# Kernel tuning notes

Measured on AMD Instinct MI355X. Metric: run time of the kernel, lower is better.

## Reference

```python
import jax, jax.numpy as jnp
import numpy as np


def fft_conv(u, k):
    # u: (b, d, l) signal, k: (d, l) per-channel filter
    # Causal (linear) convolution via zero-padded FFT of size 2*l.
    # Matches torch fft_conv: rfft(k)/n * rfft(u), irfft(norm='forward')
    # which nets out to the standard unnormalized-forward / 1/n-inverse pair.
    seqlen = u.shape[-1]
    fft_size = 2 * seqlen
    k_f = jnp.fft.rfft(k, n=fft_size)            # (d, fft_size//2+1) complex
    u_f = jnp.fft.rfft(u, n=fft_size)            # (b, d, fft_size//2+1)
    y = jnp.fft.irfft(u_f * k_f, n=fft_size)[..., :seqlen]
    return y


def setup_inputs() -> dict:
    key = jax.random.key(0)
    k1, k2 = jax.random.split(key)
    b, l, d = 4, 8192, 1024
    x = jax.random.normal(k1, (b, l, d), dtype=jnp.float32)
    filt = jax.random.normal(k2, (d, l), dtype=jnp.float32)  # nn.Parameter(d_model, l_max)
    return {"x": x, "filt": filt}


def reference(x, filt):
    # x: (b, l, d) -> transpose to (b, d, l), fft conv, transpose back
    u = jnp.swapaxes(x, 1, 2)
    y = fft_conv(u, filt)
    y = jnp.swapaxes(y, 1, 2)
    return y.astype(x.dtype)
```

## Files before the change

### kernel.cpp

```cpp
#include <hip/hip_runtime.h>


#define M 8192
#define NTH 256
#define MAXP 17

__device__ __forceinline__ float2 cadd(float2 a, float2 b){ return make_float2(a.x+b.x, a.y+b.y); }
__device__ __forceinline__ float2 csub(float2 a, float2 b){ return make_float2(a.x-b.x, a.y-b.y); }
__device__ __forceinline__ float2 cmul(float2 a, float2 b){ return make_float2(a.x*b.x - a.y*b.y, a.x*b.y + a.y*b.x); }
__device__ __forceinline__ float2 conjf2(float2 a){ return make_float2(a.x, -a.y); }
__device__ __forceinline__ int rev13(int k){ return (int)(__brev((unsigned)k) >> 19); }
__device__ __forceinline__ int swz(int e){ return e ^ ((e >> 4) & 15) ^ ((e >> 8) & 15); }

static __device__ const float PI_F = 3.14159265358979323846f;

constexpr float CR_C[17] = {
  1.f, 0.98078528f, 0.92387953f, 0.83146961f, 0.70710678f,
  0.55557023f, 0.38268343f, 0.19509032f, 0.f, -0.19509032f,
  -0.38268343f, -0.55557023f, -0.70710678f, -0.83146961f,
  -0.92387953f, -0.98078528f, -1.f };
constexpr float CR_S[17] = {
  0.f, 0.19509032f, 0.38268343f, 0.55557023f, 0.70710678f,
  0.83146961f, 0.92387953f, 0.98078528f, 1.f, 0.98078528f,
  0.92387953f, 0.83146961f, 0.70710678f, 0.55557023f,
  0.38268343f, 0.19509032f, 0.f };

__device__ __forceinline__ float2 cmul_cr(float2 a, int idx, bool inv) {
  if (idx == 0) return a;
  const float c = CR_C[idx], s = CR_S[idx];
  if (!inv) return make_float2(a.x*c + a.y*s, a.y*c - a.x*s);
  return make_float2(a.x*c - a.y*s, a.x*s + a.y*c);
}

template<int HS, bool INV, bool FIRST_PAD, bool LAST_HALF>
__device__ __forceinline__ void fft5_regs(float2 (&p)[32], int r) {
  float s, c;
  const float th = PI_F * (float)r * (1.0f / (16.0f * (float)HS));
  __sincosf(INV ? th : -th, &s, &c);
  float2 w[5];
  w[0] = make_float2(c, s);
  w[1] = cmul(w[0], w[0]);
  w[2] = cmul(w[1], w[1]);
  w[3] = cmul(w[2], w[2]);
  w[4] = cmul(w[3], w[3]);
  if (!INV) {
#pragma unroll
    for (int st = 0; st < 5; ++st) {
      const int D = 16 >> st;
#pragma unroll
      for (int t0 = 0; t0 < 32; ++t0) {
        if ((t0 & D) == 0) {
          const int u = t0 & (D - 1);
          float2 a = p[t0];
          if (FIRST_PAD && st == 0) {
            p[t0 + D] = cmul_cr(cmul(a, w[0]), u, false);
          } else {
            float2 b = p[t0 + D];
            p[t0] = cadd(a, b);
            p[t0 + D] = cmul_cr(cmul(csub(a, b), w[st]), u * (16 / D), false);
          }
        }
      }
    }
  } else {
#pragma unroll
    for (int st = 0; st < 5; ++st) {
      const int D = 1 << st;
#pragma unroll
      for (int t0 = 0; t0 < 32; ++t0) {
        if ((t0 & D) == 0) {
          const int u = t0 & (D - 1);
          float2 b = cmul_cr(cmul(p[t0 + D], w[4 - st]), u * (16 / D), true);
          float2 a = p[t0];
          p[t0] = cadd(a, b);
          if (!(LAST_HALF && st == 4)) p[t0 + D] = csub(a, b);
        }
      }
    }
  }
}

template<int HS, bool INV>
__device__ __forceinline__ void pass5_lds(float2* L, int tid) {
  const int r = tid & (HS - 1);
  const int base = ((tid - r) << 5) + r;
  float2 p[32];
#pragma unroll
  for (int t = 0; t < 32; ++t) p[t] = L[swz(base + t * HS)];
  fft5_regs<HS, INV, false, false>(p, r);
#pragma unroll
  for (int t = 0; t < 32; ++t) L[swz(base + t * HS)] = p[t];
}

template<bool INV>
__device__ __forceinline__ void pass3_lds(float2* L, int tid) {
#pragma unroll
  for (int g = 0; g < 4; ++g) {
    const int base = tid * 32 + g * 8;
    float2 p[8];
#pragma unroll
    for (int t = 0; t < 8; ++t) p[t] = L[swz(base + t)];
    if (!INV) {
#pragma unroll
      for (int st = 0; st < 3; ++st) {
        const int D = 4 >> st;
#pragma unroll
        for (int t0 = 0; t0 < 8; ++t0) {
          if ((t0 & D) == 0) {
            const int u = t0 & (D - 1);
            float2 a = p[t0], b = p[t0 + D];
            p[t0] = cadd(a, b);
            p[t0 + D] = cmul_cr(csub(a, b), u * (16 / D), false);
          }
        }
      }
    } else {
#pragma unroll
      for (int st = 0; st < 3; ++st) {
        const int D = 1 << st;
#pragma unroll
        for (int t0 = 0; t0 < 8; ++t0) {
          if ((t0 & D) == 0) {
            const int u = t0 & (D - 1);
            float2 b = cmul_cr(p[t0 + D], u * (16 / D), true);
            float2 a = p[t0];
            p[t0] = cadd(a, b);
            p[t0 + D] = csub(a, b);
          }
        }
      }
    }
#pragma unroll
    for (int t = 0; t < 8; ++t) L[swz(base + t)] = p[t];
  }
}

__global__ __launch_bounds__(NTH, 2)
void filt_fft_kernel(const float* __restrict__ filt, float4* __restrict__ kf) {
  __shared__ float2 L[M];
  const int tid = threadIdx.x;
  const int d = blockIdx.x;
  const float* fp = filt + (size_t)d * 8192;
  {
    float2 p[32];
#pragma unroll
    for (int t = 0; t < 16; ++t) {
      int m = tid + t * NTH;
      p[t] = make_float2(fp[2*m], fp[2*m + 1]);
    }
#pragma unroll
    for (int t = 16; t < 32; ++t) p[t] = make_float2(0.f, 0.f);
    fft5_regs<256, false, true, false>(p, tid);
#pragma unroll
    for (int t = 0; t < 32; ++t) L[swz(tid + t * 256)] = p[t];
  }
  __syncthreads();
  pass5_lds<8, false>(L, tid);
  __syncthreads();
  pass3_lds<false>(L, tid);
  __syncthreads();
  float4* out = kf + (size_t)d * (M/2 + 1);
  for (int k = tid; k <= M/2; k += NTH) {
    int rk  = rev13(k);
    int rmk = rev13((M - k) & (M - 1));
    float2 Zk = L[swz(rk)], Zmk = L[swz(rmk)];
    float2 Ze = make_float2(0.5f*(Zk.x + Zmk.x), 0.5f*(Zk.y - Zmk.y));
    float2 t  = make_float2(Zk.x - Zmk.x, Zk.y + Zmk.y);
    float2 Zo = make_float2(0.5f*t.y, -0.5f*t.x);
    float s, c; __sincosf(-PI_F * (float)k * (1.0f/(float)M), &s, &c);
    float2 W = make_float2(c, s);
    float2 WZo = cmul(W, Zo);
    float2 Kk = cadd(Ze, WZo);
    float2 Km = conjf2(csub(Ze, WZo));
    out[k] = make_float4(Kk.x, Kk.y, Km.x, Km.y);
  }
}

__global__ __launch_bounds__(NTH, 2)
void longconv_kf_kernel(const float* __restrict__ x,
                        const float4* __restrict__ kf,
                        float* __restrict__ y) {
  __shared__ float2 L[M];
  const int tid = threadIdx.x;

  const int nwg = gridDim.x;
  const int cpx = nwg >> 3;
  const int bid = blockIdx.x;
  const int blk = (bid & 7) * cpx + (bid >> 3);
  const int d = blk & 1023;
  const int b = blk >> 10;

  {
    const float* xp = x + (size_t)b * (8192 * 1024) + d;
    float2 p[32];
#pragma unroll
    for (int t = 0; t < 16; ++t) {
      int m = tid + t * NTH;
      p[t] = make_float2(xp[(size_t)(2*m)     * 1024],
                         xp[(size_t)(2*m + 1) * 1024]);
    }
#pragma unroll
    for (int t = 16; t < 32; ++t) p[t] = make_float2(0.f, 0.f);
    fft5_regs<256, false, true, false>(p, tid);
#pragma unroll
    for (int t = 0; t < 32; ++t) L[swz(tid + t * 256)] = p[t];
  }
  __syncthreads();
  pass5_lds<8, false>(L, tid);
  __syncthreads();
  pass3_lds<false>(L, tid);
  __syncthreads();

  {
    const float4* kfp = kf + (size_t)d * (M/2 + 1);
#pragma unroll
    for (int pq = 0; pq < MAXP; ++pq) {
      int k = tid + pq * NTH;
      if (k <= M/2) {
        float4 kv = kfp[k];
        int rk  = rev13(k);
        int rmk = rev13((M - k) & (M - 1));
        float2 Zk = L[swz(rk)], Zmk = L[swz(rmk)];
        float2 Ze = make_float2(0.5f*(Zk.x + Zmk.x), 0.5f*(Zk.y - Zmk.y));
        float2 t  = make_float2(Zk.x - Zmk.x, Zk.y + Zmk.y);
        float2 Zo = make_float2(0.5f*t.y, -0.5f*t.x);
        float s, c; __sincosf(-PI_F * (float)k * (1.0f/(float)M), &s, &c);
        float2 W = make_float2(c, s);
        float2 WZo = cmul(W, Zo);
        float2 Uk  = cadd(Ze, WZo);
        float2 Umk = conjf2(csub(Ze, WZo));
        float2 Yk  = cmul(Uk,  make_float2(kv.x, kv.y));
        float2 Ymk = cmul(Umk, make_float2(kv.z, kv.w));
        float2 Ye  = make_float2(0.5f*(Yk.x + Ymk.x), 0.5f*(Yk.y - Ymk.y));
        float2 t2  = make_float2(0.5f*(Yk.x - Ymk.x), 0.5f*(Yk.y + Ymk.y));
        float2 Zoy = cmul(conjf2(W), t2);
        float2 Zyk  = make_float2(Ye.x - Zoy.y, Ye.y + Zoy.x);
        float2 Zymk = make_float2(Ye.x + Zoy.y, Zoy.x - Ye.y);
        L[swz(rk)]  = Zyk;
        L[swz(rmk)] = Zymk;
      }
    }
  }
  __syncthreads();

  pass3_lds<true>(L, tid);
  __syncthreads();
  pass5_lds<8, true>(L, tid);
  __syncthreads();

  {
    float2 p[32];
#pragma unroll
    for (int t = 0; t < 32; ++t) p[t] = L[swz(tid + t * 256)];
    fft5_regs<256, true, false, true>(p, tid);
    float* yp = y + (size_t)b * (8192 * 1024) + d;
    const float inv = 1.0f / (float)M;
#pragma unroll
    for (int t = 0; t < 16; ++t) {
      int m = tid + t * NTH;
      yp[(size_t)(2*m)     * 1024] = p[t].x * inv;
      yp[(size_t)(2*m + 1) * 1024] = p[t].y * inv;
    }
  }
}

__global__ __launch_bounds__(NTH, 2)
void longconv_fallback_kernel(const float* __restrict__ x,
                              const float* __restrict__ filt,
                              float* __restrict__ y) {
  __shared__ float2 L[M];
  const int tid = threadIdx.x;
  const int nwg = gridDim.x;
  const int cpx = nwg >> 3;
  const int bid = blockIdx.x;
  const int blk = (bid & 7) * cpx + (bid >> 3);
  const int d = blk & 1023;
  const int b = blk >> 10;

  float2 Kk[MAXP], Kmk[MAXP];

  {
    const float* fp = filt + (size_t)d * 8192;
    float2 p[32];
#pragma unroll
    for (int t = 0; t < 16; ++t) {
      int m = tid + t * NTH;
      p[t] = make_float2(fp[2*m], fp[2*m + 1]);
    }
#pragma unroll
    for (int t = 16; t < 32; ++t) p[t] = make_float2(0.f, 0.f);
    fft5_regs<256, false, true, false>(p, tid);
#pragma unroll
    for (int t = 0; t < 32; ++t) L[swz(tid + t * 256)] = p[t];
  }
  __syncthreads();
  pass5_lds<8, false>(L, tid);
  __syncthreads();
  pass3_lds<false>(L, tid);
  __syncthreads();
#pragma unroll
  for (int pq = 0; pq < MAXP; ++pq) {
    int k = tid + pq * NTH;
    if (k <= M/2) {
      int rk  = rev13(k);
      int rmk = rev13((M - k) & (M - 1));
      float2 Zk = L[swz(rk)], Zmk = L[swz(rmk)];
      float2 Ze = make_float2(0.5f*(Zk.x + Zmk.x), 0.5f*(Zk.y - Zmk.y));
      float2 t  = make_float2(Zk.x - Zmk.x, Zk.y + Zmk.y);
      float2 Zo = make_float2(0.5f*t.y, -0.5f*t.x);
      float s, c; __sincosf(-PI_F * (float)k * (1.0f/(float)M), &s, &c);
      float2 W = make_float2(c, s);
      float2 WZo = cmul(W, Zo);
      Kk[pq]  = cadd(Ze, WZo);
      Kmk[pq] = conjf2(csub(Ze, WZo));
    }
  }
  __syncthreads();

  {
    const float* xp = x + (size_t)b * (8192 * 1024) + d;
    float2 p[32];
#pragma unroll
    for (int t = 0; t < 16; ++t) {
      int m = tid + t * NTH;
      p[t] = make_float2(xp[(size_t)(2*m)     * 1024],
                         xp[(size_t)(2*m + 1) * 1024]);
    }
#pragma unroll
    for (int t = 16; t < 32; ++t) p[t] = make_float2(0.f, 0.f);
    fft5_regs<256, false, true, false>(p, tid);
#pragma unroll
    for (int t = 0; t < 32; ++t) L[swz(tid + t * 256)] = p[t];
  }
  __syncthreads();
  pass5_lds<8, false>(L, tid);
  __syncthreads();
  pass3_lds<false>(L, tid);
  __syncthreads();

#pragma unroll
  for (int pq = 0; pq < MAXP; ++pq) {
    int k = tid + pq * NTH;
    if (k <= M/2) {
      int rk  = rev13(k);
      int rmk = rev13((M - k) & (M - 1));
      float2 Zk = L[swz(rk)], Zmk = L[swz(rmk)];
      float2 Ze = make_float2(0.5f*(Zk.x + Zmk.x), 0.5f*(Zk.y - Zmk.y));
      float2 t  = make_float2(Zk.x - Zmk.x, Zk.y + Zmk.y);
      float2 Zo = make_float2(0.5f*t.y, -0.5f*t.x);
      float s, c; __sincosf(-PI_F * (float)k * (1.0f/(float)M), &s, &c);
      float2 W = make_float2(c, s);
      float2 WZo = cmul(W, Zo);
      float2 Uk  = cadd(Ze, WZo);
      float2 Umk = conjf2(csub(Ze, WZo));
      float2 Yk  = cmul(Uk,  Kk[pq]);
      float2 Ymk = cmul(Umk, Kmk[pq]);
      float2 Ye  = make_float2(0.5f*(Yk.x + Ymk.x), 0.5f*(Yk.y - Ymk.y));
      float2 t2  = make_float2(0.5f*(Yk.x - Ymk.x), 0.5f*(Yk.y + Ymk.y));
      float2 Zoy = cmul(conjf2(W), t2);
      float2 Zyk  = make_float2(Ye.x - Zoy.y, Ye.y + Zoy.x);
      float2 Zymk = make_float2(Ye.x + Zoy.y, Zoy.x - Ye.y);
      L[swz(rk)]  = Zyk;
      L[swz(rmk)] = Zymk;
    }
  }
  __syncthreads();

  pass3_lds<true>(L, tid);
  __syncthreads();
  pass5_lds<8, true>(L, tid);
  __syncthreads();

  {
    float2 p[32];
#pragma unroll
    for (int t = 0; t < 32; ++t) p[t] = L[swz(tid + t * 256)];
    fft5_regs<256, true, false, true>(p, tid);
    float* yp = y + (size_t)b * (8192 * 1024) + d;
    const float inv = 1.0f / (float)M;
#pragma unroll
    for (int t = 0; t < 16; ++t) {
      int m = tid + t * NTH;
      yp[(size_t)(2*m)     * 1024] = p[t].x * inv;
      yp[(size_t)(2*m + 1) * 1024] = p[t].y * inv;
    }
  }
}

extern "C" void kernel_launch(void* const* d_in, const int* in_sizes, int n_in,
                              void* d_out, int out_size, void* d_ws, size_t ws_size,
                              hipStream_t stream) {
  const float* x    = (const float*)d_in[0];
  const float* filt = (const float*)d_in[1];
  float* y = (float*)d_out;

  const int D = 1024, Lseq = 8192;
  const int B = in_sizes[0] / (D * Lseq);

  const size_t kf_bytes = (size_t)D * (M/2 + 1) * sizeof(float4);
  dim3 grid(B * D), block(NTH);

  if (d_ws != nullptr && ws_size >= kf_bytes) {
    hipLaunchKernelGGL(filt_fft_kernel, dim3(D), dim3(NTH), 0, stream,
                       filt, (float4*)d_ws);
    hipLaunchKernelGGL(longconv_kf_kernel, grid, block, 0, stream,
                       x, (const float4*)d_ws, y);
  } else {
    hipLaunchKernelGGL(longconv_fallback_kernel, grid, block, 0, stream,
                       x, filt, y);
  }
}
```

Measured before the change: 620.6 us.

## Split LDS FFT stage into two half-size batches to halve shared memory

```diff
diff --git a/kernel.cpp b/kernel.cpp
--- a/kernel.cpp
+++ b/kernel.cpp
@@ -80,16 +80,262 @@
   }
 }
 
-template<int HS, bool INV>
+template<bool INV>
+__device__ __forceinline__ void fft4_regs(float2 (&p)[16], float2 w0) {
+  float2 w[4];
+  w[0] = w0;
+  w[1] = cmul(w[0], w[0]);
+  w[2] = cmul(w[1], w[1]);
+  w[3] = cmul(w[2], w[2]);
+  if (!INV) {
+#pragma unroll
+    for (int st = 0; st < 4; ++st) {
+      const int D = 8 >> st;
+#pragma unroll
+      for (int t0 = 0; t0 < 16; ++t0) {
+        if ((t0 & D) == 0) {
+          const int u = t0 & (D - 1);
+          float2 a = p[t0], b = p[t0 + D];
+          p[t0] = cadd(a, b);
+          p[t0 + D] = cmul_cr(cmul(csub(a, b), w[st]), u * (16 / D), false);
+        }
+      }
+    }
+  } else {
+#pragma unroll
+    for (int st = 0; st < 4; ++st) {
+      const int D = 1 << st;
+#pragma unroll
+      for (int t0 = 0; t0 < 16; ++t0) {
+        if ((t0 & D) == 0) {
+          const int u = t0 & (D - 1);
+          float2 b = cmul_cr(cmul(p[t0 + D], w[3 - st]), u * (16 / D), true);
+          float2 a = p[t0];
+          p[t0] = cadd(a, b);
+          p[t0 + D] = csub(a, b);
+        }
+      }
+    }
+  }
+}
+
+template<bool INV>
+__device__ __forceinline__ void fft4c_regs(float2 (&p)[16]) {
+  if (!INV) {
+#pragma unroll
+    for (int st = 0; st < 4; ++st) {
+      const int D = 8 >> st;
+#pragma unroll
+      for (int t0 = 0; t0 < 16; ++t0) {
+        if ((t0 & D) == 0) {
+          const int u = t0 & (D - 1);
+          float2 a = p[t0], b = p[t0 + D];
+          p[t0] = cadd(a, b);
+          p[t0 + D] = cmul_cr(csub(a, b), u * (16 / D), false);
+        }
+      }
+    }
+  } else {
+#pragma unroll
+    for (int st = 0; st < 4; ++st) {
+      const int D = 1 << st;
+#pragma unroll
+      for (int t0 = 0; t0 < 16; ++t0) {
+        if ((t0 & D) == 0) {
+          const int u = t0 & (D - 1);
+          float2 b = cmul_cr(p[t0 + D], u * (16 / D), true);
+          float2 a = p[t0];
+          p[t0] = cadd(a, b);
+          p[t0 + D] = csub(a, b);
+        }
+      }
+    }
+  }
+}
+
+template<bool INV>
+__device__ __forceinline__ void pass_s16(float2* LB, int tid) {
+  const int r = tid & 15, gl = tid >> 4;
+  const int base = gl * 256 + r;
+  float2 q[16];
+#pragma unroll
+  for (int t = 0; t < 16; ++t) q[t] = LB[swz(base + 16 * t)];
+  float s, c;
+  const float th = PI_F * (float)r * (1.0f / 128.0f);
+  __sincosf(INV ? th : -th, &s, &c);
+  fft4_regs<INV>(q, make_float2(c, s));
+#pragma unroll
+  for (int t = 0; t < 16; ++t) LB[swz(base + 16 * t)] = q[t];
+}
+
+template<bool INV>
+__device__ __forceinline__ void pass_c16(float2* LB, int tid) {
+  const int base = tid * 16;
+  float2 q[16];
+#pragma unroll
+  for (int t = 0; t < 16; ++t) q[t] = LB[swz(base + t)];
+  fft4c_regs<INV>(q);
+#pragma unroll
+  for (int t = 0; t < 16; ++t) LB[swz(base + t)] = q[t];
+}
+
+template<int HALF>
+__device__ __forceinline__ void conv_batch(float2* LB, float2 (&p)[32],
+                                           int tid, const float4* kfp) {
+#pragma unroll
+  for (int g = 0; g < 16; ++g) LB[swz(g * 256 + tid)] = p[HALF * 16 + g];
+  __syncthreads();
+  pass_s16<false>(LB, tid);
+  __syncthreads();
+  pass_c16<false>(LB, tid);
+  __syncthreads();
+  constexpr int NQ = (HALF == 0) ? 9 : 8;
+#pragma unroll
+  for (int q = 0; q < NQ; ++q) {
+    int kp = tid + 256 * q;
+    int k = 2 * kp + HALF;
+    if (k <= M / 2) {
+      float4 kv = kfp[k];
+      int rk  = rev13(k) - HALF * 4096;
+      int rmk = rev13((M - k) & (M - 1)) - HALF * 4096;
+      float2 Zk = LB[swz(rk)], Zmk = LB[swz(rmk)];
+      float2 Ze = make_float2(0.5f*(Zk.x + Zmk.x), 0.5f*(Zk.y - Zmk.y));
+      float2 t  = make_float2(Zk.x - Zmk.x, Zk.y + Zmk.y);
+      float2 Zo = make_float2(0.5f*t.y, -0.5f*t.x);
+      float s, c; __sincosf(-PI_F * (float)k * (1.0f/(float)M), &s, &c);
+      float2 W = make_float2(c, s);
+      float2 WZo = cmul(W, Zo);
+      float2 Uk  = cadd(Ze, WZo);
+      float2 Umk = conjf2(csub(Ze, WZo));
+      float2 Yk  = cmul(Uk,  make_float2(kv.x, kv.y));
+      float2 Ymk = cmul(Umk, make_float2(kv.z, kv.w));
+      float2 Ye  = make_float2(0.5f*(Yk.x + Ymk.x), 0.5f*(Yk.y - Ymk.y));
+      float2 t2  = make_float2(0.5f*(Yk.x - Ymk.x), 0.5f*(Yk.y + Ymk.y));
+      float2 Zoy = cmul(conjf2(W), t2);
+      float2 Zyk  = make_float2(Ye.x - Zoy.y, Ye.y + Zoy.x);
+      float2 Zymk = make_float2(Ye.x + Zoy.y, Zoy.x - Ye.y);
+      LB[swz(rk)]  = Zyk;
+      LB[swz(rmk)] = Zymk;
+    }
+  }
+  __syncthreads();
+  pass_c16<true>(LB, tid);
+  __syncthreads();
+  pass_s16<true>(LB, tid);
+  __syncthreads();
+#pragma unroll
+  for (int g = 0; g < 16; ++g) p[HALF * 16 + g] = LB[swz(g * 256 + tid)];
+  __syncthreads();
+}
+
+template<int HALF>
+__device__ __forceinline__ void filt_batch(float2* LB, float2 (&p)[32],
+                                           int tid, float4* out) {
+#pragma unroll
+  for (int g = 0; g < 16; ++g) LB[swz(g * 256 + tid)] = p[HALF * 16 + g];
+  __syncthreads();
+  pass_s16<false>(LB, tid);
+  __syncthreads();
+  pass_c16<false>(LB, tid);
+  __syncthreads();
+  constexpr int NQ = (HALF == 0) ? 9 : 8;
+#pragma unroll
+  for (int q = 0; q < NQ; ++q) {
+    int kp = tid + 256 * q;
+    int k = 2 * kp + HALF;
+    if (k <= M / 2) {
+      int rk  = rev13(k) - HALF * 4096;
+      int rmk = rev13((M - k) & (M - 1)) - HALF * 4096;
+      float2 Zk = LB[swz(rk)], Zmk = LB[swz(rmk)];
+      float2 Ze = make_float2(0.5f*(Zk.x + Zmk.x), 0.5f*(Zk.y - Zmk.y));
+      float2 t  = make_float2(Zk.x - Zmk.x, Zk.y + Zmk.y);
+      float2 Zo = make_float2(0.5f*t.y, -0.5f*t.x);
+      float s, c; __sincosf(-PI_F * (float)k * (1.0f/(float)M), &s, &c);
+      float2 W = make_float2(c, s);
+      float2 WZo = cmul(W, Zo);
+      float2 Kk = cadd(Ze, WZo);
+      float2 Km = conjf2(csub(Ze, WZo));
+      out[k] = make_float4(Kk.x, Kk.y, Km.x, Km.y);
+    }
+  }
+  __syncthreads();
+}
+
+__global__ __launch_bounds__(NTH, 4)
+void filt_fft_kernel(const float* __restrict__ filt, float4* __restrict__ kf) {
+  __shared__ float2 LB[4096];
+  const int tid = threadIdx.x;
+  const int d = blockIdx.x;
+  const float* fp = filt + (size_t)d * 8192;
+  float2 p[32];
+#pragma unroll
+  for (int t = 0; t < 16; ++t) {
+    int m = tid + t * NTH;
+    p[t] = make_float2(fp[2*m], fp[2*m + 1]);
+  }
+#pragma unroll
+  for (int t = 16; t < 32; ++t) p[t] = make_float2(0.f, 0.f);
+  fft5_regs<256, false, true, false>(p, tid);
+  float4* out = kf + (size_t)d * (M/2 + 1);
+  filt_batch<0>(LB, p, tid, out);
+  filt_batch<1>(LB, p, tid, out);
+}
+
+__global__ __launch_bounds__(NTH, 4)
+void longconv_kf_kernel(const float* __restrict__ x,
+                        const float4* __restrict__ kf,
+                        float* __restrict__ y) {
+  __shared__ float2 LB[4096];
+  const int tid = threadIdx.x;
+
+  const int nwg = gridDim.x;
+  const int cpx = nwg >> 3;
+  const int bid = blockIdx.x;
+  const int blk = (bid & 7) * cpx + (bid >> 3);
+  const int d = blk & 1023;
+  const int b = blk >> 10;
+
+  float2 p[32];
+  {
+    const float* xp = x + (size_t)b * (8192 * 1024) + d;
+#pragma unroll
+    for (int t = 0; t < 16; ++t) {
+      int m = tid + t * NTH;
+      p[t] = make_float2(xp[(size_t)(2*m)     * 1024],
+                         xp[(size_t)(2*m + 1) * 1024]);
+    }
+#pragma unroll
+    for (int t = 16; t < 32; ++t) p[t] = make_float2(0.f, 0.f);
+    fft5_regs<256, false, true, false>(p, tid);
+  }
+
+  const float4* kfp = kf + (size_t)d * (M/2 + 1);
+  conv_batch<0>(LB, p, tid, kfp);
+  conv_batch<1>(LB, p, tid, kfp);
+
+  {
+    fft5_regs<256, true, false, true>(p, tid);
+    float* yp = y + (size_t)b * (8192 * 1024) + d;
+    const float inv = 1.0f / (float)M;
+#pragma unroll
+    for (int t = 0; t < 16; ++t) {
+      int m = tid + t * NTH;
+      yp[(size_t)(2*m)     * 1024] = p[t].x * inv;
+      yp[(size_t)(2*m + 1) * 1024] = p[t].y * inv;
+    }
+  }
+}
+
+template<bool INV>
 __device__ __forceinline__ void pass5_lds(float2* L, int tid) {
-  const int r = tid & (HS - 1);
+  const int r = tid & 7;
   const int base = ((tid - r) << 5) + r;
   float2 p[32];
 #pragma unroll
-  for (int t = 0; t < 32; ++t) p[t] = L[swz(base + t * HS)];
-  fft5_regs<HS, INV, false, false>(p, r);
-#pragma unroll
-  for (int t = 0; t < 32; ++t) L[swz(base + t * HS)] = p[t];
+  for (int t = 0; t < 32; ++t) p[t] = L[swz(base + t * 8)];
+  fft5_regs<8, INV, false, false>(p, r);
+#pragma unroll
+  for (int t = 0; t < 32; ++t) L[swz(base + t * 8)] = p[t];
 }
 
 template<bool INV>
@@ -132,135 +378,6 @@
     }
 #pragma unroll
     for (int t = 0; t < 8; ++t) L[swz(base + t)] = p[t];
-  }
-}
-
-__global__ __launch_bounds__(NTH, 2)
-void filt_fft_kernel(const float* __restrict__ filt, float4* __restrict__ kf) {
-  __shared__ float2 L[M];
-  const int tid = threadIdx.x;
-  const int d = blockIdx.x;
-  const float* fp = filt + (size_t)d * 8192;
-  {
-    float2 p[32];
-#pragma unroll
-    for (int t = 0; t < 16; ++t) {
-      int m = tid + t * NTH;
-      p[t] = make_float2(fp[2*m], fp[2*m + 1]);
-    }
-#pragma unroll
-    for (int t = 16; t < 32; ++t) p[t] = make_float2(0.f, 0.f);
-    fft5_regs<256, false, true, false>(p, tid);
-#pragma unroll
-    for (int t = 0; t < 32; ++t) L[swz(tid + t * 256)] = p[t];
-  }
-  __syncthreads();
-  pass5_lds<8, false>(L, tid);
-  __syncthreads();
-  pass3_lds<false>(L, tid);
-  __syncthreads();
-  float4* out = kf + (size_t)d * (M/2 + 1);
-  for (int k = tid; k <= M/2; k += NTH) {
-    int rk  = rev13(k);
-    int rmk = rev13((M - k) & (M - 1));
-    float2 Zk = L[swz(rk)], Zmk = L[swz(rmk)];
-    float2 Ze = make_float2(0.5f*(Zk.x + Zmk.x), 0.5f*(Zk.y - Zmk.y));
-    float2 t  = make_float2(Zk.x - Zmk.x, Zk.y + Zmk.y);
-    float2 Zo = make_float2(0.5f*t.y, -0.5f*t.x);
-    float s, c; __sincosf(-PI_F * (float)k * (1.0f/(float)M), &s, &c);
-    float2 W = make_float2(c, s);
-    float2 WZo = cmul(W, Zo);
-    float2 Kk = cadd(Ze, WZo);
-    float2 Km = conjf2(csub(Ze, WZo));
-    out[k] = make_float4(Kk.x, Kk.y, Km.x, Km.y);
-  }
-}
-
-__global__ __launch_bounds__(NTH, 2)
-void longconv_kf_kernel(const float* __restrict__ x,
-                        const float4* __restrict__ kf,
-                        float* __restrict__ y) {
-  __shared__ float2 L[M];
-  const int tid = threadIdx.x;
-
-  const int nwg = gridDim.x;
-  const int cpx = nwg >> 3;
-  const int bid = blockIdx.x;
-  const int blk = (bid & 7) * cpx + (bid >> 3);
-  const int d = blk & 1023;
-  const int b = blk >> 10;
-
-  {
-    const float* xp = x + (size_t)b * (8192 * 1024) + d;
-    float2 p[32];
-#pragma unroll
-    for (int t = 0; t < 16; ++t) {
-      int m = tid + t * NTH;
-      p[t] = make_float2(xp[(size_t)(2*m)     * 1024],
-                         xp[(size_t)(2*m + 1) * 1024]);
-    }
-#pragma unroll
-    for (int t = 16; t < 32; ++t) p[t] = make_float2(0.f, 0.f);
-    fft5_regs<256, false, true, false>(p, tid);
-#pragma unroll
-    for (int t = 0; t < 32; ++t) L[swz(tid + t * 256)] = p[t];
-  }
-  __syncthreads();
-  pass5_lds<8, false>(L, tid);
-  __syncthreads();
-  pass3_lds<false>(L, tid);
-  __syncthreads();
-
-  {
-    const float4* kfp = kf + (size_t)d * (M/2 + 1);
-#pragma unroll
-    for (int pq = 0; pq < MAXP; ++pq) {
-      int k = tid + pq * NTH;
-      if (k <= M/2) {
-        float4 kv = kfp[k];
-        int rk  = rev13(k);
-        int rmk = rev13((M - k) & (M - 1));
-        float2 Zk = L[swz(rk)], Zmk = L[swz(rmk)];
-        float2 Ze = make_float2(0.5f*(Zk.x + Zmk.x), 0.5f*(Zk.y - Zmk.y));
-        float2 t  = make_float2(Zk.x - Zmk.x, Zk.y + Zmk.y);
-        float2 Zo = make_float2(0.5f*t.y, -0.5f*t.x);
-        float s, c; __sincosf(-PI_F * (float)k * (1.0f/(float)M), &s, &c);
-        float2 W = make_float2(c, s);
-        float2 WZo = cmul(W, Zo);
-        float2 Uk  = cadd(Ze, WZo);
-        float2 Umk = conjf2(csub(Ze, WZo));
-        float2 Yk  = cmul(Uk,  make_float2(kv.x, kv.y));
-        float2 Ymk = cmul(Umk, make_float2(kv.z, kv.w));
-        float2 Ye  = make_float2(0.5f*(Yk.x + Ymk.x), 0.5f*(Yk.y - Ymk.y));
-        float2 t2  = make_float2(0.5f*(Yk.x - Ymk.x), 0.5f*(Yk.y + Ymk.y));
-        float2 Zoy = cmul(conjf2(W), t2);
-        float2 Zyk  = make_float2(Ye.x - Zoy.y, Ye.y + Zoy.x);
-        float2 Zymk = make_float2(Ye.x + Zoy.y, Zoy.x - Ye.y);
-        L[swz(rk)]  = Zyk;
-        L[swz(rmk)] = Zymk;
-      }
-    }
-  }
-  __syncthreads();
-
-  pass3_lds<true>(L, tid);
-  __syncthreads();
-  pass5_lds<8, true>(L, tid);
-  __syncthreads();
-
-  {
-    float2 p[32];
-#pragma unroll
-    for (int t = 0; t < 32; ++t) p[t] = L[swz(tid + t * 256)];
-    fft5_regs<256, true, false, true>(p, tid);
-    float* yp = y + (size_t)b * (8192 * 1024) + d;
-    const float inv = 1.0f / (float)M;
-#pragma unroll
-    for (int t = 0; t < 16; ++t) {
-      int m = tid + t * NTH;
-      yp[(size_t)(2*m)     * 1024] = p[t].x * inv;
-      yp[(size_t)(2*m + 1) * 1024] = p[t].y * inv;
-    }
   }
 }
 
@@ -294,7 +411,7 @@
     for (int t = 0; t < 32; ++t) L[swz(tid + t * 256)] = p[t];
   }
   __syncthreads();
-  pass5_lds<8, false>(L, tid);
+  pass5_lds<false>(L, tid);
   __syncthreads();
   pass3_lds<false>(L, tid);
   __syncthreads();
@@ -333,7 +450,7 @@
     for (int t = 0; t < 32; ++t) L[swz(tid + t * 256)] = p[t];
   }
   __syncthreads();
-  pass5_lds<8, false>(L, tid);
+  pass5_lds<false>(L, tid);
   __syncthreads();
   pass3_lds<false>(L, tid);
   __syncthreads();
@@ -368,7 +485,7 @@
 
   pass3_lds<true>(L, tid);
   __syncthreads();
-  pass5_lds<8, true>(L, tid);
+  pass5_lds<true>(L, tid);
   __syncthreads();
 
   {
```

After: 847.1 us. 36.5% more time.
